# Optimization experiments

Measured on AMD Instinct MI355X. Metric: run time of the kernel, lower is better.

## Reference

```python
import jax, jax.numpy as jnp
import numpy as np

T, B, I, H, O = 2048, 128, 32, 128, 1


def setup_inputs() -> dict:
    key = jax.random.key(0)
    ks = jax.random.split(key, 5)
    X = jax.random.normal(ks[0], (T, B, I), dtype=jnp.float32)
    W_in = jax.random.normal(ks[1], (H, I), dtype=jnp.float32) / np.sqrt(I)
    W_hh = jax.random.normal(ks[2], (H, H), dtype=jnp.float32) / np.sqrt(H)
    rnn_bias = jnp.zeros((H,), dtype=jnp.float32)
    alpha = jax.random.uniform(ks[3], (H,), dtype=jnp.float32)
    value_W = jax.random.normal(ks[4], (O, H), dtype=jnp.float32) / np.sqrt(H)
    value_bias = jnp.zeros((O,), dtype=jnp.float32)
    return {"X": X, "W_in": W_in, "W_hh": W_hh, "rnn_bias": rnn_bias,
            "alpha": alpha, "value_W": value_W, "value_bias": value_bias}


def reference(X, W_in, W_hh, rnn_bias, alpha, value_W, value_bias):
    # X: (T, B, I). Precompute input projections for all timesteps at once.
    xproj = jnp.einsum('tbi,hi->tbh', X, W_in)  # (T, B, H)

    def step(h_prev, xp_t):
        h_tilde = jnp.tanh(xp_t + h_prev @ W_hh.T + rnn_bias)
        h = (1.0 - alpha) * h_prev + alpha * h_tilde  # per-unit leaky blend
        return h, h

    h0 = jnp.zeros((X.shape[1], W_hh.shape[0]), dtype=X.dtype)
    last_hidden, Z = jax.lax.scan(step, h0, xproj)  # Z: (T, B, H)
    V = value_bias + jnp.einsum('tbh,oh->tbo', Z, value_W)  # (T, B, O)
    return V, last_hidden
```

## Files before the change

### kernel.cpp

```cpp
#include <hip/hip_runtime.h>

#define TT 2048
#define BB 128
#define II 32
#define HH 128
#define NW (TT / 8)

typedef float v2f __attribute__((ext_vector_type(2)));
typedef float v4f __attribute__((ext_vector_type(4)));
typedef unsigned int u32;
typedef __attribute__((address_space(3))) u32 lds_u32;
typedef const __attribute__((address_space(1))) u32 glb_u32;

__device__ __forceinline__ v2f pk_fma(v2f a, v2f b, v2f c) {
    v2f d;
    asm("v_pk_fma_f32 %0, %1, %2, %3" : "=v"(d) : "v"(a), "v"(b), "v"(c));
    return d;
}

template <int CTRL>
__device__ __forceinline__ float dpp_mov(float p) {
    return __int_as_float(__builtin_amdgcn_update_dpp(0, __float_as_int(p), CTRL, 0xF, 0xF, true));
}
template <int CTRL>
__device__ __forceinline__ float dpp_add(float p) {
    return p + dpp_mov<CTRL>(p);
}

__global__ __launch_bounds__(512)
void vrnn_kernel(const float* __restrict__ X, const float* __restrict__ W_in,
                 const float* __restrict__ W_hh, const float* __restrict__ rnn_bias,
                 const float* __restrict__ alpha, const float* __restrict__ value_W,
                 const float* __restrict__ value_bias, float* __restrict__ out)
{
    const int b    = blockIdx.x;
    const int tid  = threadIdx.x;
    const int wave = tid >> 6;
    const int lane = tid & 63;
    const int g    = lane >> 4;
    const int j    = lane & 15;
    const int base = 16 * wave + 4 * g;

    __shared__ __align__(16) float xw[2][8][II];
    __shared__ __align__(16) float gbuf[2][192];

    if (wave == 0) {
        const float* src = X + (size_t)(lane >> 3) * (BB * II) + b * II + (lane & 7) * 4;
        __builtin_amdgcn_global_load_lds((glb_u32*)src, (lds_u32*)(&xw[0][0][0]), 16, 0, 0);
    }

    v2f a_c[4], vwc[4];
#pragma unroll
    for (int i = 0; i < 4; ++i) {
        a_c[i] = *(const v2f*)(alpha   + 8 * j + 2 * i);
        vwc[i] = *(const v2f*)(value_W + 8 * j + 2 * i);
    }
    v2f m1[4][4], m2[4][4], wi[4], binit[4];
#pragma unroll
    for (int r = 0; r < 4; ++r) {
        const float* wr = W_hh + (size_t)(base + r) * HH + 8 * j;
#pragma unroll
        for (int i = 0; i < 4; ++i) {
            v2f w2 = *(const v2f*)(wr + 2 * i);
            m2[r][i] = w2 * a_c[i];
            m1[r][i] = w2 - m2[r][i];
        }
        wi[r]    = *(const v2f*)(W_in + (size_t)(base + r) * II + 2 * j);
        binit[r] = (v2f){ (j == 0) ? rnn_bias[base + r] : 0.0f, 0.0f };
    }
    const float vb = value_bias[0];
    const int  hrow  = base + j;
    const int  gwoff = 12 * (hrow >> 3) + (hrow & 7);

    v2f hc[4], a1[4];
#pragma unroll
    for (int i = 0; i < 4; ++i) hc[i] = (v2f){0.f, 0.f};
#pragma unroll
    for (int r = 0; r < 4; ++r) a1[r] = binit[r];

    if (tid < 192) gbuf[1][tid] = 0.0f;
    __syncthreads();

    float* outV = out;
    float* outH = out + (size_t)TT * BB;

    for (int w = 0; w < NW; ++w) {
        if (wave == 0 && w + 1 < NW) {
            const float* src = X + (size_t)((w + 1) * 8 + (lane >> 3)) * (BB * II)
                                 + b * II + (lane & 7) * 4;
            __builtin_amdgcn_global_load_lds((glb_u32*)src,
                (lds_u32*)(&xw[(w + 1) & 1][0][0]), 16, 0, 0);
        }
#pragma unroll
        for (int s = 0; s < 8; ++s) {
            const int par = s & 1;
            const float* gb = &gbuf[par ^ 1][12 * j];
            const v4f g0 = *(const v4f*)(gb);
            const v4f g1 = *(const v4f*)(gb + 4);
            v2f gp[4] = { (v2f){g0.x, g0.y}, (v2f){g0.z, g0.w},
                          (v2f){g1.x, g1.y}, (v2f){g1.z, g1.w} };
            const v2f xc = *(const v2f*)(&xw[w & 1][s][2 * j]);
            float p0, p1, p2, p3;
            {
                v2f a;
                a = pk_fma(wi[0], xc, a1[0]);
                a = pk_fma(m2[0][0], gp[0], a); a = pk_fma(m2[0][1], gp[1], a);
                a = pk_fma(m2[0][2], gp[2], a); a = pk_fma(m2[0][3], gp[3], a);
                p0 = a.x + a.y;
                a = pk_fma(wi[1], xc, a1[1]);
                a = pk_fma(m2[1][0], gp[0], a); a = pk_fma(m2[1][1], gp[1], a);
                a = pk_fma(m2[1][2], gp[2], a); a = pk_fma(m2[1][3], gp[3], a);
                p1 = a.x + a.y;
                a = pk_fma(wi[2], xc, a1[2]);
                a = pk_fma(m2[2][0], gp[0], a); a = pk_fma(m2[2][1], gp[1], a);
                a = pk_fma(m2[2][2], gp[2], a); a = pk_fma(m2[2][3], gp[3], a);
                p2 = a.x + a.y;
                a = pk_fma(wi[3], xc, a1[3]);
                a = pk_fma(m2[3][0], gp[0], a); a = pk_fma(m2[3][1], gp[1], a);
                a = pk_fma(m2[3][2], gp[2], a); a = pk_fma(m2[3][3], gp[3], a);
                p3 = a.x + a.y;
            }
            const bool b0 = (j & 1) != 0;
            const bool b1 = (j & 2) != 0;
            float rA = (b0 ? p1 : p0) + dpp_mov<0xB1>(b0 ? p0 : p1);
            float rB = (b0 ? p3 : p2) + dpp_mov<0xB1>(b0 ? p2 : p3);
            float pre = (b1 ? rB : rA) + dpp_mov<0x4E>(b1 ? rA : rB);
            pre = dpp_add<0x124>(pre);
            pre = dpp_add<0x128>(pre);
            const float e  = __builtin_amdgcn_exp2f(pre * 2.8853900817779268f);
            const float rc = __builtin_amdgcn_rcpf(e + 1.0f);
            const float gt = fmaf(-2.0f, rc, 1.0f);
            if (j < 4) gbuf[par][gwoff] = gt;
#pragma unroll
            for (int i = 0; i < 4; ++i) hc[i] = pk_fma(a_c[i], gp[i] - hc[i], hc[i]);
            v2f vt = vwc[0] * hc[0];
            vt = pk_fma(vwc[1], hc[1], vt);
            vt = pk_fma(vwc[2], hc[2], vt);
            vt = pk_fma(vwc[3], hc[3], vt);
            float vsum = vt.x + vt.y;
            vsum = dpp_add<0xB1>(vsum); vsum = dpp_add<0x4E>(vsum);
            vsum = dpp_add<0x124>(vsum); vsum = dpp_add<0x128>(vsum);
            if (wave == s && lane == 0 && (w + s) != 0)
                outV[(size_t)(8 * w + s - 1) * BB + b] = vb + vsum;
#pragma unroll
            for (int r = 0; r < 4; ++r) {
                v2f a = binit[r];
                a = pk_fma(m1[r][0], hc[0], a); a = pk_fma(m1[r][1], hc[1], a);
                a = pk_fma(m1[r][2], hc[2], a); a = pk_fma(m1[r][3], hc[3], a);
                a1[r] = a;
            }
            if (wave == 0 && s == 7)
                asm volatile("s_waitcnt vmcnt(0)" ::: "memory");
            asm volatile("s_waitcnt lgkmcnt(0)" ::: "memory");
            __builtin_amdgcn_s_barrier();
            __builtin_amdgcn_sched_barrier(0);
        }
    }

    {
        const float* gb = &gbuf[(TT - 1) & 1][12 * j];
        const v4f g0 = *(const v4f*)(gb);
        const v4f g1 = *(const v4f*)(gb + 4);
        v2f gp[4] = { (v2f){g0.x, g0.y}, (v2f){g0.z, g0.w},
                      (v2f){g1.x, g1.y}, (v2f){g1.z, g1.w} };
#pragma unroll
        for (int i = 0; i < 4; ++i) hc[i] = pk_fma(a_c[i], gp[i] - hc[i], hc[i]);
        v2f vt = vwc[0] * hc[0];
        vt = pk_fma(vwc[1], hc[1], vt);
        vt = pk_fma(vwc[2], hc[2], vt);
        vt = pk_fma(vwc[3], hc[3], vt);
        float vsum = vt.x + vt.y;
        vsum = dpp_add<0xB1>(vsum); vsum = dpp_add<0x4E>(vsum);
        vsum = dpp_add<0x124>(vsum); vsum = dpp_add<0x128>(vsum);
        if (wave == 0 && lane == 0)
            outV[(size_t)(TT - 1) * BB + b] = vb + vsum;
        if (wave == 0 && g == 0) {
#pragma unroll
            for (int i = 0; i < 4; ++i)
                *(v2f*)(outH + (size_t)b * HH + 8 * j + 2 * i) = hc[i];
        }
    }
}

extern "C" void kernel_launch(void* const* d_in, const int* in_sizes, int n_in,
                              void* d_out, int out_size, void* d_ws, size_t ws_size,
                              hipStream_t stream) {
    const float* X      = (const float*)d_in[0];
    const float* W_in   = (const float*)d_in[1];
    const float* W_hh   = (const float*)d_in[2];
    const float* rbias  = (const float*)d_in[3];
    const float* alpha  = (const float*)d_in[4];
    const float* vW     = (const float*)d_in[5];
    const float* vbias  = (const float*)d_in[6];
    float* out = (float*)d_out;

    vrnn_kernel<<<dim3(BB), dim3(512), 0, stream>>>(X, W_in, W_hh, rbias, alpha, vW, vbias, out);
}
```

Measured before the change: 871.0 us.

## Halve block to 4 waves, each lane owning 8 hidden rows and updating h directly

Each block now runs 256 threads, and each 16-lane group computes 8 rows of the W_hh matvec instead of 4. The reduction tree gains a row-shift DPP stage. The leaky blend is now done per owning lane on the new hidden state, and h (rather than the tanh output) is shared through LDS, which removes the algebraic split of W_hh into alpha-weighted halves and the replicated per-lane h update. Fewer waves means a cheaper per-step barrier, at the cost of doing twice as many FMAs per lane on the serial critical path.

```diff
diff --git a/kernel.cpp b/kernel.cpp
--- a/kernel.cpp
+++ b/kernel.cpp
@@ -26,8 +26,14 @@
 __device__ __forceinline__ float dpp_add(float p) {
     return p + dpp_mov<CTRL>(p);
 }
+template <int CTRL>
+__device__ __forceinline__ float pair_red(float x, float y, bool sel) {
+    float keep = sel ? y : x;
+    float give = sel ? x : y;
+    return keep + dpp_mov<CTRL>(give);
+}
 
-__global__ __launch_bounds__(512)
+__global__ __launch_bounds__(256)
 void vrnn_kernel(const float* __restrict__ X, const float* __restrict__ W_in,
                  const float* __restrict__ W_hh, const float* __restrict__ rnn_bias,
                  const float* __restrict__ alpha, const float* __restrict__ value_W,
@@ -39,46 +45,40 @@
     const int lane = tid & 63;
     const int g    = lane >> 4;
     const int j    = lane & 15;
-    const int base = 16 * wave + 4 * g;
+    const int base = 32 * wave + 8 * g;
+    const int rown = base + (j & 7);
 
     __shared__ __align__(16) float xw[2][8][II];
-    __shared__ __align__(16) float gbuf[2][192];
+    __shared__ __align__(16) float hbuf[2][192];
 
     if (wave == 0) {
         const float* src = X + (size_t)(lane >> 3) * (BB * II) + b * II + (lane & 7) * 4;
         __builtin_amdgcn_global_load_lds((glb_u32*)src, (lds_u32*)(&xw[0][0][0]), 16, 0, 0);
     }
 
-    v2f a_c[4], vwc[4];
+    v2f wh[8][4], wi8[8], binit[8];
 #pragma unroll
-    for (int i = 0; i < 4; ++i) {
-        a_c[i] = *(const v2f*)(alpha   + 8 * j + 2 * i);
-        vwc[i] = *(const v2f*)(value_W + 8 * j + 2 * i);
-    }
-    v2f m1[4][4], m2[4][4], wi[4], binit[4];
-#pragma unroll
-    for (int r = 0; r < 4; ++r) {
+    for (int r = 0; r < 8; ++r) {
         const float* wr = W_hh + (size_t)(base + r) * HH + 8 * j;
-#pragma unroll
-        for (int i = 0; i < 4; ++i) {
-            v2f w2 = *(const v2f*)(wr + 2 * i);
-            m2[r][i] = w2 * a_c[i];
-            m1[r][i] = w2 - m2[r][i];
-        }
-        wi[r]    = *(const v2f*)(W_in + (size_t)(base + r) * II + 2 * j);
+        v4f a0 = *(const v4f*)(wr);
+        v4f a1 = *(const v4f*)(wr + 4);
+        wh[r][0] = (v2f){a0.x, a0.y}; wh[r][1] = (v2f){a0.z, a0.w};
+        wh[r][2] = (v2f){a1.x, a1.y}; wh[r][3] = (v2f){a1.z, a1.w};
+        wi8[r]   = *(const v2f*)(W_in + (size_t)(base + r) * II + 2 * j);
         binit[r] = (v2f){ (j == 0) ? rnn_bias[base + r] : 0.0f, 0.0f };
     }
-    const float vb = value_bias[0];
-    const int  hrow  = base + j;
-    const int  gwoff = 12 * (hrow >> 3) + (hrow & 7);
+    v2f vwc[4];
+#pragma unroll
+    for (int i = 0; i < 4; ++i) vwc[i] = *(const v2f*)(value_W + 8 * j + 2 * i);
+    const float al_own = alpha[rown];
+    const float vb     = value_bias[0];
+    const bool  b0 = (j & 1) != 0;
+    const bool  b1 = (j & 2) != 0;
+    const bool  b2 = (j & 4) != 0;
+    const int   woff = 12 * (4 * wave + g) + (j & 7);
+    float hreg = 0.0f;
 
-    v2f hc[4], a1[4];
-#pragma unroll
-    for (int i = 0; i < 4; ++i) hc[i] = (v2f){0.f, 0.f};
-#pragma unroll
-    for (int r = 0; r < 4; ++r) a1[r] = binit[r];
-
-    if (tid < 192) gbuf[1][tid] = 0.0f;
+    if (tid < 192) hbuf[1][tid] = 0.0f;
     __syncthreads();
 
     float* outV = out;
@@ -94,92 +94,85 @@
 #pragma unroll
         for (int s = 0; s < 8; ++s) {
             const int par = s & 1;
-            const float* gb = &gbuf[par ^ 1][12 * j];
-            const v4f g0 = *(const v4f*)(gb);
-            const v4f g1 = *(const v4f*)(gb + 4);
-            v2f gp[4] = { (v2f){g0.x, g0.y}, (v2f){g0.z, g0.w},
-                          (v2f){g1.x, g1.y}, (v2f){g1.z, g1.w} };
+            const float* hb = &hbuf[par ^ 1][12 * j];
+            const v4f h0 = *(const v4f*)(hb);
+            const v4f h1 = *(const v4f*)(hb + 4);
+            v2f hp[4] = { (v2f){h0.x, h0.y}, (v2f){h0.z, h0.w},
+                          (v2f){h1.x, h1.y}, (v2f){h1.z, h1.w} };
             const v2f xc = *(const v2f*)(&xw[w & 1][s][2 * j]);
-            float p0, p1, p2, p3;
-            {
-                v2f a;
-                a = pk_fma(wi[0], xc, a1[0]);
-                a = pk_fma(m2[0][0], gp[0], a); a = pk_fma(m2[0][1], gp[1], a);
-                a = pk_fma(m2[0][2], gp[2], a); a = pk_fma(m2[0][3], gp[3], a);
-                p0 = a.x + a.y;
-                a = pk_fma(wi[1], xc, a1[1]);
-                a = pk_fma(m2[1][0], gp[0], a); a = pk_fma(m2[1][1], gp[1], a);
-                a = pk_fma(m2[1][2], gp[2], a); a = pk_fma(m2[1][3], gp[3], a);
-                p1 = a.x + a.y;
-                a = pk_fma(wi[2], xc, a1[2]);
-                a = pk_fma(m2[2][0], gp[0], a); a = pk_fma(m2[2][1], gp[1], a);
-                a = pk_fma(m2[2][2], gp[2], a); a = pk_fma(m2[2][3], gp[3], a);
-                p2 = a.x + a.y;
-                a = pk_fma(wi[3], xc, a1[3]);
-                a = pk_fma(m2[3][0], gp[0], a); a = pk_fma(m2[3][1], gp[1], a);
-                a = pk_fma(m2[3][2], gp[2], a); a = pk_fma(m2[3][3], gp[3], a);
-                p3 = a.x + a.y;
+            float p[8];
+#pragma unroll
+            for (int r = 0; r < 8; ++r) {
+                v2f a = pk_fma(wi8[r], xc, binit[r]);
+                a = pk_fma(wh[r][0], hp[0], a);
+                a = pk_fma(wh[r][1], hp[1], a);
+                a = pk_fma(wh[r][2], hp[2], a);
+                a = pk_fma(wh[r][3], hp[3], a);
+                p[r] = a.x + a.y;
             }
-            const bool b0 = (j & 1) != 0;
-            const bool b1 = (j & 2) != 0;
-            float rA = (b0 ? p1 : p0) + dpp_mov<0xB1>(b0 ? p0 : p1);
-            float rB = (b0 ? p3 : p2) + dpp_mov<0xB1>(b0 ? p2 : p3);
-            float pre = (b1 ? rB : rA) + dpp_mov<0x4E>(b1 ? rA : rB);
-            pre = dpp_add<0x124>(pre);
-            pre = dpp_add<0x128>(pre);
+            float q0 = pair_red<0xB1>(p[0], p[1], b0);
+            float q1 = pair_red<0xB1>(p[2], p[3], b0);
+            float q2 = pair_red<0xB1>(p[4], p[5], b0);
+            float q3 = pair_red<0xB1>(p[6], p[7], b0);
+            float r0 = pair_red<0x4E>(q0, q1, b1);
+            float r1 = pair_red<0x4E>(q2, q3, b1);
+            const float k3  = b2 ? r1 : r0;
+            const float g3  = b2 ? r0 : r1;
+            const float vL  = dpp_mov<0x104>(g3);
+            const float vR  = dpp_mov<0x114>(g3);
+            float pre = k3 + (b2 ? vR : vL);
+            pre += dpp_mov<0x128>(pre);
             const float e  = __builtin_amdgcn_exp2f(pre * 2.8853900817779268f);
             const float rc = __builtin_amdgcn_rcpf(e + 1.0f);
             const float gt = fmaf(-2.0f, rc, 1.0f);
-            if (j < 4) gbuf[par][gwoff] = gt;
-#pragma unroll
-            for (int i = 0; i < 4; ++i) hc[i] = pk_fma(a_c[i], gp[i] - hc[i], hc[i]);
-            v2f vt = vwc[0] * hc[0];
-            vt = pk_fma(vwc[1], hc[1], vt);
-            vt = pk_fma(vwc[2], hc[2], vt);
-            vt = pk_fma(vwc[3], hc[3], vt);
-            float vsum = vt.x + vt.y;
-            vsum = dpp_add<0xB1>(vsum); vsum = dpp_add<0x4E>(vsum);
-            vsum = dpp_add<0x124>(vsum); vsum = dpp_add<0x128>(vsum);
-            if (wave == s && lane == 0 && (w + s) != 0)
-                outV[(size_t)(8 * w + s - 1) * BB + b] = vb + vsum;
-#pragma unroll
-            for (int r = 0; r < 4; ++r) {
-                v2f a = binit[r];
-                a = pk_fma(m1[r][0], hc[0], a); a = pk_fma(m1[r][1], hc[1], a);
-                a = pk_fma(m1[r][2], hc[2], a); a = pk_fma(m1[r][3], hc[3], a);
-                a1[r] = a;
+            hreg = fmaf(al_own, gt - hreg, hreg);
+            hbuf[par][woff] = hreg;
+            if (wave == (s & 3)) {
+                if ((w | s) != 0) {
+                    v2f vt = vwc[0] * hp[0];
+                    vt = pk_fma(vwc[1], hp[1], vt);
+                    vt = pk_fma(vwc[2], hp[2], vt);
+                    vt = pk_fma(vwc[3], hp[3], vt);
+                    float vs = vt.x + vt.y;
+                    vs = dpp_add<0xB1>(vs);
+                    vs = dpp_add<0x4E>(vs);
+                    const float uL = dpp_mov<0x104>(vs);
+                    const float uR = dpp_mov<0x114>(vs);
+                    vs += b2 ? uR : uL;
+                    vs = dpp_add<0x128>(vs);
+                    if (lane == 0)
+                        outV[(size_t)(8 * w + s - 1) * BB + b] = vb + vs;
+                }
             }
             if (wave == 0 && s == 7)
                 asm volatile("s_waitcnt vmcnt(0)" ::: "memory");
             asm volatile("s_waitcnt lgkmcnt(0)" ::: "memory");
             __builtin_amdgcn_s_barrier();
-            __builtin_amdgcn_sched_barrier(0);
         }
     }
 
-    {
-        const float* gb = &gbuf[(TT - 1) & 1][12 * j];
-        const v4f g0 = *(const v4f*)(gb);
-        const v4f g1 = *(const v4f*)(gb + 4);
-        v2f gp[4] = { (v2f){g0.x, g0.y}, (v2f){g0.z, g0.w},
-                      (v2f){g1.x, g1.y}, (v2f){g1.z, g1.w} };
-#pragma unroll
-        for (int i = 0; i < 4; ++i) hc[i] = pk_fma(a_c[i], gp[i] - hc[i], hc[i]);
-        v2f vt = vwc[0] * hc[0];
-        vt = pk_fma(vwc[1], hc[1], vt);
-        vt = pk_fma(vwc[2], hc[2], vt);
-        vt = pk_fma(vwc[3], hc[3], vt);
-        float vsum = vt.x + vt.y;
-        vsum = dpp_add<0xB1>(vsum); vsum = dpp_add<0x4E>(vsum);
-        vsum = dpp_add<0x124>(vsum); vsum = dpp_add<0x128>(vsum);
-        if (wave == 0 && lane == 0)
-            outV[(size_t)(TT - 1) * BB + b] = vb + vsum;
-        if (wave == 0 && g == 0) {
-#pragma unroll
-            for (int i = 0; i < 4; ++i)
-                *(v2f*)(outH + (size_t)b * HH + 8 * j + 2 * i) = hc[i];
-        }
+    if (wave == 0) {
+        const float* hb = &hbuf[1][12 * j];
+        const v4f h0 = *(const v4f*)(hb);
+        const v4f h1 = *(const v4f*)(hb + 4);
+        v2f hp[4] = { (v2f){h0.x, h0.y}, (v2f){h0.z, h0.w},
+                      (v2f){h1.x, h1.y}, (v2f){h1.z, h1.w} };
+        v2f vt = vwc[0] * hp[0];
+        vt = pk_fma(vwc[1], hp[1], vt);
+        vt = pk_fma(vwc[2], hp[2], vt);
+        vt = pk_fma(vwc[3], hp[3], vt);
+        float vs = vt.x + vt.y;
+        vs = dpp_add<0xB1>(vs);
+        vs = dpp_add<0x4E>(vs);
+        const float uL = dpp_mov<0x104>(vs);
+        const float uR = dpp_mov<0x114>(vs);
+        vs += b2 ? uR : uL;
+        vs = dpp_add<0x128>(vs);
+        if (lane == 0)
+            outV[(size_t)(TT - 1) * BB + b] = vb + vs;
     }
+    if (j < 8)
+        outH[(size_t)b * HH + base + j] = hreg;
 }
 
 extern "C" void kernel_launch(void* const* d_in, const int* in_sizes, int n_in,
@@ -194,5 +187,5 @@
     const float* vbias  = (const float*)d_in[6];
     float* out = (float*)d_out;
 
-    vrnn_kernel<<<dim3(BB), dim3(512), 0, stream>>>(X, W_in, W_hh, rbias, alpha, vW, vbias, out);
+    vrnn_kernel<<<dim3(BB), dim3(256), 0, stream>>>(X, W_in, W_hh, rbias, alpha, vW, vbias, out);
 }
```

Measured after the change: 792.8 us. 9.0% less time.
